# Optimization experiments

Hardware: AMD Instinct MI355X
Metric: run time of the kernel (lower is better)

Reference implementation:

```python
import jax, jax.numpy as jnp
import numpy as np

B, T, D, S, K = 4, 4096, 1024, 2048, 8

def _l2norm(v, axis=-1, eps=1e-12):
    # matches torch F.normalize: v / max(||v||, eps)
    n = jnp.sqrt(jnp.sum(v * v, axis=axis, keepdims=True))
    return v / jnp.maximum(n, eps)

def setup_inputs() -> dict:
    key = jax.random.key(0)
    ks = jax.random.split(key, 9)
    H = D // 2
    return {
        "x": jax.random.normal(ks[0], (B, T, D), dtype=jnp.float32),
        "memory_keys": jax.random.normal(ks[1], (S, D), dtype=jnp.float32) * 0.02,
        "memory_values": jax.random.normal(ks[2], (S, D), dtype=jnp.float32) * 0.02,
        "Wq": jax.random.normal(ks[3], (D, D), dtype=jnp.float32) * (1.0 / np.sqrt(D)),
        "Wo": jax.random.normal(ks[4], (D, D), dtype=jnp.float32) * (1.0 / np.sqrt(D)),
        "gW1": jax.random.normal(ks[5], (H, 2 * D), dtype=jnp.float32) * (1.0 / np.sqrt(2 * D)),
        "gb1": jnp.zeros((H,), dtype=jnp.float32),
        "gW2": jax.random.normal(ks[6], (1, H), dtype=jnp.float32) * (1.0 / np.sqrt(H)),
        "gb2": jnp.zeros((1,), dtype=jnp.float32),
    }

def reference(x, memory_keys, memory_values, Wq, Wo, gW1, gb1, gW2, gb2):
    # query projection (Linear, no bias): y = x @ W.T
    queries = jnp.einsum('btd,ed->bte', x, Wq)
    keys_norm = _l2norm(memory_keys)          # [S, D]
    queries_norm = _l2norm(queries)           # [B, T, D]
    # cosine similarities [B, T, S]
    sims = jnp.einsum('btd,sd->bts', queries_norm, keys_norm)
    topk_sims, topk_idx = jax.lax.top_k(sims, K)      # [B, T, K]
    topk_w = jax.nn.softmax(topk_sims, axis=-1)       # [B, T, K]
    topk_vals = memory_values[topk_idx]               # [B, T, K, D]
    retrieved = jnp.einsum('btk,btkd->btd', topk_w, topk_vals)
    retrieved = jnp.einsum('btd,ed->bte', retrieved, Wo)
    gate_in = jnp.concatenate([x, retrieved], axis=-1)           # [B, T, 2D]
    h = jax.nn.gelu(jnp.einsum('btc,hc->bth', gate_in, gW1) + gb1, approximate=False)
    gate = jax.nn.sigmoid(jnp.einsum('bth,oh->bto', h, gW2) + gb2)  # [B, T, 1]
    return x + gate * retrieved
```

## Files before the change

### kernel.cpp

```cpp
#include <hip/hip_runtime.h>
#include <math.h>

#define NROWS 16384
#define DDIM  1024
#define SKEYS 2048
#define KTOP  8
#define HDIM  512

typedef short  s16x8 __attribute__((ext_vector_type(8)));
typedef float  f32x4 __attribute__((ext_vector_type(4)));

#define GL16(g, l) __builtin_amdgcn_global_load_lds(                      \
    (const __attribute__((address_space(1))) void*)(g),                   \
    (__attribute__((address_space(3))) void*)(l), 16, 0, 0)

__device__ __forceinline__ float wave_sum(float v) {
#pragma unroll
    for (int off = 32; off > 0; off >>= 1) v += __shfl_xor(v, off, 64);
    return v;
}

__device__ __forceinline__ unsigned short f2bf(float f) {
    union { float f; unsigned u; } c; c.f = f;
    unsigned u = c.u;
    unsigned r = (u + 0x7FFFu + ((u >> 16) & 1u)) >> 16;
    return (unsigned short)r;
}

__device__ __forceinline__ float gelu_exact(float v) {
    return 0.5f * v * (1.0f + erff(v * 0.7071067811865475f));
}

__device__ __forceinline__ ushort4 cvt4(float4 v) {
    ushort4 o;
    o.x = f2bf(v.x); o.y = f2bf(v.y); o.z = f2bf(v.z); o.w = f2bf(v.w);
    return o;
}

__global__ __launch_bounds__(256) void prep_kernel(
        const float* __restrict__ x,   const float* __restrict__ Wq,
        const float* __restrict__ Wo,  const float* __restrict__ mv,
        const float* __restrict__ gW1, const float* __restrict__ mk,
        unsigned short* __restrict__ x_bf, unsigned short* __restrict__ bcat,
        unsigned short* __restrict__ wqT, unsigned short* __restrict__ wo_bf,
        unsigned short* __restrict__ mv_bf, unsigned short* __restrict__ gw1b,
        unsigned short* __restrict__ kn) {
    int bid = blockIdx.x, t = threadIdx.x;
    __shared__ float tlds[64][65];
    {
        float4 v = ((const float4*)(mk + (size_t)bid * DDIM))[t];
        float ss = v.x * v.x + v.y * v.y + v.z * v.z + v.w * v.w;
        ss = wave_sum(ss);
        __shared__ float wsum[4];
        if ((t & 63) == 0) wsum[t >> 6] = ss;
        __syncthreads();
        float tot = wsum[0] + wsum[1] + wsum[2] + wsum[3];
        float sc = 1.0f / fmaxf(sqrtf(tot), 1e-12f);
        float4 o = make_float4(v.x * sc, v.y * sc, v.z * sc, v.w * sc);
        ((ushort4*)(kn + (size_t)bid * DDIM))[t] = cvt4(o);
    }
    if (bid < 256) {
        int d0 = (bid >> 4) * 64, e0 = (bid & 15) * 64;
#pragma unroll
        for (int i = 0; i < 16; ++i) {
            int dr = i * 4 + (t >> 6);
            tlds[dr][t & 63] = Wq[(size_t)(d0 + dr) * DDIM + e0 + (t & 63)];
        }
        __syncthreads();
#pragma unroll
        for (int i = 0; i < 16; ++i) {
            int er = i * 4 + (t >> 6);
            wqT[(size_t)(e0 + er) * DDIM + d0 + (t & 63)] = f2bf(tlds[t & 63][er]);
        }
    }
    int gid = bid * 256 + t, stride = gridDim.x * 256;
    for (int i = gid; i < NROWS * DDIM / 4; i += stride)
        ((ushort4*)x_bf)[i] = cvt4(((const float4*)x)[i]);
    for (int i = gid; i < DDIM * DDIM / 4; i += stride)
        ((ushort4*)bcat)[524288 + i] = cvt4(((const float4*)Wq)[i]);
    for (int i = gid; i < HDIM * 2 * DDIM / 4; i += stride) {
        float4 v = ((const float4*)gW1)[i];
        int r = i >> 9, c4 = i & 511;
        if (c4 < 256) ((ushort4*)bcat)[786432 + r * 256 + c4] = cvt4(v);
        else          ((ushort4*)gw1b)[r * 256 + (c4 - 256)] = cvt4(v);
    }
    for (int i = gid; i < DDIM * DDIM / 4; i += stride)
        ((ushort4*)wo_bf)[i] = cvt4(((const float4*)Wo)[i]);
    for (int i = gid; i < SKEYS * DDIM / 4; i += stride)
        ((ushort4*)mv_bf)[i] = cvt4(((const float4*)mv)[i]);
}

struct GArg {
    const unsigned short* A;
    const unsigned short* B;
    unsigned short* C;
    unsigned short* C2;
    float* qpart;
    int Ncols, N2cols, nsplit, nsplit2, gx, nblocks, mode;
};

__global__ __launch_bounds__(256, 3) void dualgemm(GArg g0, GArg g1, int split) {
    __shared__ __align__(16) unsigned short As[2][4096];
    __shared__ __align__(16) unsigned short Bs[2][4096];

    int tid = threadIdx.x, l = tid & 63, wid = tid >> 6;
    bool first = ((int)blockIdx.x < split);
    GArg g = first ? g0 : g1;
    int bid = first ? blockIdx.x : blockIdx.x - split;
    int cpx = g.nblocks >> 3;
    int sbid = (bid & 7) * cpx + (bid >> 3);
    int m0 = (sbid / g.gx) * 128;
    int n0 = (sbid % g.gx) * 128;

    int wr = wid >> 1, wc = wid & 1;
    constexpr int NT = 32;

    f32x4 acc[4][4];
#pragma unroll
    for (int i = 0; i < 4; ++i)
#pragma unroll
        for (int j = 0; j < 4; ++j) acc[i][j] = (f32x4){0.f, 0.f, 0.f, 0.f};

    int srow   = tid >> 2;
    int schunk = (tid & 3) ^ ((srow >> 1) & 3);
    int offA[2], offB[2];
#pragma unroll
    for (int i = 0; i < 2; ++i) {
        offA[i] = (m0 + i * 64 + srow) * 1024;
        offB[i] = (n0 + i * 64 + srow) * 1024;
    }
    int ldsU = wid * 512;

#define STAGE(bsel, kt_)                                                       \
    do {                                                                       \
        int gk_ = (kt_) * 32 + schunk * 8;                                     \
        _Pragma("unroll")                                                      \
        for (int i_ = 0; i_ < 2; ++i_) {                                       \
            GL16(g.A + offA[i_] + gk_, &As[bsel][i_ * 2048 + ldsU]);           \
            GL16(g.B + offB[i_] + gk_, &Bs[bsel][i_ * 2048 + ldsU]);           \
        }                                                                      \
    } while (0)

    STAGE(0, 0);

    int frow = l & 15;
    int fp   = (l >> 4) ^ ((frow >> 1) & 3);
    int aoff = (wr * 64 + frow) * 32 + fp * 8;
    int boff = (wc * 64 + frow) * 32 + fp * 8;

#pragma unroll 2
    for (int kt = 0; kt < NT; ++kt) {
        int b = kt & 1;
        if (kt + 1 < NT) {
            STAGE(b ^ 1, kt + 1);
            asm volatile("s_waitcnt vmcnt(4)" ::: "memory");
        } else {
            asm volatile("s_waitcnt vmcnt(0)" ::: "memory");
        }
        __builtin_amdgcn_s_barrier();
        asm volatile("" ::: "memory");

        s16x8 af[4], bfr[4];
#pragma unroll
        for (int mf = 0; mf < 4; ++mf)
            af[mf] = *(const s16x8*)&As[b][aoff + mf * 512];
#pragma unroll
        for (int nf = 0; nf < 4; ++nf)
            bfr[nf] = *(const s16x8*)&Bs[b][boff + nf * 512];

        __builtin_amdgcn_s_setprio(1);
#pragma unroll
        for (int mf = 0; mf < 4; ++mf)
#pragma unroll
            for (int nf = 0; nf < 4; ++nf)
                acc[mf][nf] = __builtin_amdgcn_mfma_f32_16x16x32_bf16(
                    af[mf], bfr[nf], acc[mf][nf], 0, 0, 0);
        __builtin_amdgcn_s_setprio(0);
        asm volatile("" ::: "memory");
        __builtin_amdgcn_s_barrier();
        asm volatile("" ::: "memory");
    }
#undef STAGE

    int region = 0;
    unsigned short* cptr = g.C;
    int nc = g.Ncols, cb = n0;
    if (g.mode == 5) {
        if (n0 < g.nsplit) region = 1;
        else if (n0 < g.nsplit2) region = 2;
        else { region = 3; cptr = g.C2; nc = g.N2cols; cb = n0 - g.nsplit2; }
    }

    int crow = (l >> 4) << 2;
    int ccol = l & 15;
    if (region != 2) {
#pragma unroll
        for (int mf = 0; mf < 4; ++mf) {
            int gr = m0 + wr * 64 + mf * 16 + crow;
#pragma unroll
            for (int nf = 0; nf < 4; ++nf) {
                int gc = cb + wc * 64 + nf * 16 + ccol;
                f32x4 v = acc[mf][nf];
#pragma unroll
                for (int r2 = 0; r2 < 4; ++r2) {
                    unsigned short sv = f2bf(v[r2]);
                    if (region == 1)
                        sv = sv ^ ((sv & 0x8000) ? 0xFFFFu : 0x8000u);
                    cptr[(size_t)(gr + r2) * nc + gc] = sv;
                }
            }
        }
    } else {
        int slot = ((n0 - g.nsplit) >> 7) * 2 + wc;
#pragma unroll
        for (int mf = 0; mf < 4; ++mf)
#pragma unroll
            for (int r2 = 0; r2 < 4; ++r2) {
                float s = acc[mf][0][r2] * acc[mf][0][r2]
                        + acc[mf][1][r2] * acc[mf][1][r2]
                        + acc[mf][2][r2] * acc[mf][2][r2]
                        + acc[mf][3][r2] * acc[mf][3][r2];
                s += __shfl_xor(s, 1, 64);
                s += __shfl_xor(s, 2, 64);
                s += __shfl_xor(s, 4, 64);
                s += __shfl_xor(s, 8, 64);
                if ((l & 15) == 0)
                    g.qpart[(size_t)slot * NROWS +
                            (m0 + wr * 64 + mf * 16 + (l >> 4) * 4 + r2)] = s;
            }
    }
}

#define CED(k, i, j)                                                      \
    { unsigned mx_ = k[i] > k[j] ? k[i] : k[j];                           \
      unsigned mn_ = k[i] > k[j] ? k[j] : k[i];                           \
      k[i] = mx_; k[j] = mn_; }

__device__ __forceinline__ void sort8d(unsigned* k) {
    CED(k,0,1) CED(k,2,3) CED(k,4,5) CED(k,6,7)
    CED(k,0,2) CED(k,1,3) CED(k,4,6) CED(k,5,7)
    CED(k,1,2) CED(k,5,6)
    CED(k,0,4) CED(k,1,5) CED(k,2,6) CED(k,3,7)
    CED(k,2,4) CED(k,3,5)
    CED(k,1,2) CED(k,3,4) CED(k,5,6)
}

__device__ __forceinline__ void bclean8d(unsigned* t) {
    CED(t,0,4) CED(t,1,5) CED(t,2,6) CED(t,3,7)
    CED(t,0,2) CED(t,1,3) CED(t,4,6) CED(t,5,7)
    CED(t,0,1) CED(t,2,3) CED(t,4,5) CED(t,6,7)
}

__device__ __forceinline__ void merge8d(unsigned* a, const unsigned* b) {
    unsigned t[8];
#pragma unroll
    for (int i = 0; i < 8; ++i) t[i] = a[i] > b[7 - i] ? a[i] : b[7 - i];
    bclean8d(t);
#pragma unroll
    for (int i = 0; i < 8; ++i) a[i] = t[i];
}

__global__ __launch_bounds__(256) void mega_kernel(
        const float* __restrict__ qpart,
        const unsigned short* __restrict__ sims,
        const unsigned short* __restrict__ x_bf,
        const unsigned short* __restrict__ xg1,
        const unsigned short* __restrict__ mvo,
        const unsigned short* __restrict__ mvog,
        const float* __restrict__ gb1, const float* __restrict__ gW2,
        const float* __restrict__ gb2, float* __restrict__ out) {
    int wid = threadIdx.x >> 6, l = threadIdx.x & 63;
    int row = blockIdx.x * 4 + wid;

    const unsigned short* sr = sims + (size_t)row * SKEYS;
    uint4 raw0 = *(const uint4*)(sr + 0 * 512 + l * 8);
    uint4 raw1 = *(const uint4*)(sr + 1 * 512 + l * 8);
    uint4 raw2 = *(const uint4*)(sr + 2 * 512 + l * 8);
    uint4 raw3 = *(const uint4*)(sr + 3 * 512 + l * 8);
    const unsigned short* xr = x_bf + (size_t)row * DDIM + l * 16;
    uint4 x0 = *(const uint4*)xr, x1 = *(const uint4*)(xr + 8);
    uint4 xg = *(const uint4*)(xg1 + (size_t)row * HDIM + l * 8);

    float ssq = 0.f;
#pragma unroll
    for (int j = 0; j < 16; ++j) ssq += qpart[(size_t)j * NROWS + row];
    float qs = 1.0f / fmaxf(sqrtf(ssq), 1e-12f);

    unsigned key[32];
    {
        unsigned rw[16] = {raw0.x, raw0.y, raw0.z, raw0.w,
                           raw1.x, raw1.y, raw1.z, raw1.w,
                           raw2.x, raw2.y, raw2.z, raw2.w,
                           raw3.x, raw3.y, raw3.z, raw3.w};
#pragma unroll
        for (int c = 0; c < 4; ++c)
#pragma unroll
            for (int q2 = 0; q2 < 4; ++q2) {
                unsigned v = rw[c * 4 + q2];
                unsigned bi0 = (unsigned)(c * 512 + l * 8 + q2 * 2);
                key[c * 8 + q2 * 2]     = ((v & 0xFFFFu) << 16) | bi0;
                key[c * 8 + q2 * 2 + 1] = (v & 0xFFFF0000u) | (bi0 + 1);
            }
    }
    sort8d(key); sort8d(key + 8); sort8d(key + 16); sort8d(key + 24);
    merge8d(key, key + 8);
    merge8d(key + 16, key + 24);
    merge8d(key, key + 16);

#pragma unroll
    for (int off = 1; off <= 32; off <<= 1) {
        unsigned br[8];
#pragma unroll
        for (int i = 0; i < 8; ++i)
            br[i] = (unsigned)__shfl_xor((int)key[7 - i], off, 64);
        unsigned t[8];
#pragma unroll
        for (int i = 0; i < 8; ++i) t[i] = key[i] > br[i] ? key[i] : br[i];
        bclean8d(t);
#pragma unroll
        for (int i = 0; i < 8; ++i) key[i] = t[i];
    }

    float ov[8]; int oi[8];
#pragma unroll
    for (int j = 0; j < 8; ++j) {
        oi[j] = (int)(key[j] & 0xFFFFu);
        unsigned short ks = (unsigned short)(key[j] >> 16);
        unsigned short sv = ks ^ ((ks & 0x8000) ? 0x8000u : 0xFFFFu);
        ov[j] = __uint_as_float(((unsigned)sv) << 16);
    }
    float w[KTOP];
    float m = ov[0] * qs, ssum = 0.f;
#pragma unroll
    for (int j = 0; j < 8; ++j) { w[j] = expf(ov[j] * qs - m); ssum += w[j]; }
    float sinv = 1.0f / ssum;
#pragma unroll
    for (int j = 0; j < 8; ++j) w[j] *= sinv;

    float r2[16], hp[8];
#pragma unroll
    for (int j = 0; j < 16; ++j) r2[j] = 0.f;
#pragma unroll
    for (int j = 0; j < 8; ++j) hp[j] = 0.f;
#pragma unroll
    for (int k = 0; k < KTOP; ++k) {
        float wk = w[k];
        const unsigned short* mo = mvo + (size_t)oi[k] * DDIM + l * 16;
        uint4 a0 = *(const uint4*)mo;
        uint4 a1 = *(const uint4*)(mo + 8);
        const unsigned short* mg = mvog + (size_t)oi[k] * HDIM + l * 8;
        uint4 g0 = *(const uint4*)mg;
        unsigned aw[8] = {a0.x, a0.y, a0.z, a0.w, a1.x, a1.y, a1.z, a1.w};
#pragma unroll
        for (int j = 0; j < 8; ++j) {
            r2[2 * j]     += wk * __uint_as_float(aw[j] << 16);
            r2[2 * j + 1] += wk * __uint_as_float(aw[j] & 0xffff0000u);
        }
        unsigned gw[4] = {g0.x, g0.y, g0.z, g0.w};
#pragma unroll
        for (int j = 0; j < 4; ++j) {
            hp[2 * j]     += wk * __uint_as_float(gw[j] << 16);
            hp[2 * j + 1] += wk * __uint_as_float(gw[j] & 0xffff0000u);
        }
    }
    unsigned xgw[4] = {xg.x, xg.y, xg.z, xg.w};
    float p = 0.f;
#pragma unroll
    for (int j = 0; j < 4; ++j) {
        float h0 = gelu_exact(hp[2 * j] + __uint_as_float(xgw[j] << 16)
                              + gb1[l * 8 + 2 * j]);
        float h1 = gelu_exact(hp[2 * j + 1] + __uint_as_float(xgw[j] & 0xffff0000u)
                              + gb1[l * 8 + 2 * j + 1]);
        p += h0 * gW2[l * 8 + 2 * j] + h1 * gW2[l * 8 + 2 * j + 1];
    }
    p = wave_sum(p);
    float gate = 1.0f / (1.0f + expf(-(p + gb2[0])));
    unsigned xw[8] = {x0.x, x0.y, x0.z, x0.w, x1.x, x1.y, x1.z, x1.w};
    float o[16];
#pragma unroll
    for (int j = 0; j < 8; ++j) {
        o[2 * j]     = __uint_as_float(xw[j] << 16)         + gate * r2[2 * j];
        o[2 * j + 1] = __uint_as_float(xw[j] & 0xffff0000u) + gate * r2[2 * j + 1];
    }
    float4* po = (float4*)(out + (size_t)row * DDIM + l * 16);
    po[0] = make_float4(o[0], o[1], o[2], o[3]);
    po[1] = make_float4(o[4], o[5], o[6], o[7]);
    po[2] = make_float4(o[8], o[9], o[10], o[11]);
    po[3] = make_float4(o[12], o[13], o[14], o[15]);
}

extern "C" void kernel_launch(void* const* d_in, const int* in_sizes, int n_in,
                              void* d_out, int out_size, void* d_ws, size_t ws_size,
                              hipStream_t stream) {
    (void)in_sizes; (void)n_in; (void)out_size; (void)ws_size;
    const float* x   = (const float*)d_in[0];
    const float* mk  = (const float*)d_in[1];
    const float* mv  = (const float*)d_in[2];
    const float* Wq  = (const float*)d_in[3];
    const float* Wo  = (const float*)d_in[4];
    const float* gW1 = (const float*)d_in[5];
    const float* gb1 = (const float*)d_in[6];
    const float* gW2 = (const float*)d_in[7];
    const float* gb2 = (const float*)d_in[8];
    float* out = (float*)d_out;

    char* w = (char*)d_ws;
    unsigned short* x_bf    = (unsigned short*)w;  w += (size_t)NROWS * DDIM * 2;
    unsigned short* xg1_bf  = (unsigned short*)w;  w += (size_t)NROWS * HDIM * 2;
    unsigned short* kn_bf   = (unsigned short*)w;  w += (size_t)SKEYS * DDIM * 2;
    unsigned short* bcat    = (unsigned short*)w;  w += (size_t)3584 * DDIM * 2;
    unsigned short* wqT_bf  = (unsigned short*)w;  w += (size_t)DDIM * DDIM * 2;
    unsigned short* gw1b_bf = (unsigned short*)w;  w += (size_t)HDIM * DDIM * 2;
    unsigned short* wo_bf   = (unsigned short*)w;  w += (size_t)DDIM * DDIM * 2;
    unsigned short* mv_bf   = (unsigned short*)w;  w += (size_t)SKEYS * DDIM * 2;
    unsigned short* mvo_bf  = (unsigned short*)w;  w += (size_t)SKEYS * DDIM * 2;
    unsigned short* mvog_bf = (unsigned short*)w;  w += (size_t)SKEYS * HDIM * 2;
    unsigned short* sims    = (unsigned short*)w;  w += (size_t)NROWS * SKEYS * 2;
    float* qpart = (float*)w;                      w += (size_t)16 * NROWS * 4;

    prep_kernel<<<SKEYS, 256, 0, stream>>>(x, Wq, Wo, mv, gW1, mk,
                                           x_bf, bcat, wqT_bf, wo_bf, mv_bf,
                                           gw1b_bf, kn_bf);

    {
        GArg gk; gk.A = kn_bf; gk.B = wqT_bf; gk.C = bcat; gk.C2 = nullptr;
        gk.qpart = nullptr; gk.Ncols = DDIM; gk.N2cols = 0;
        gk.nsplit = 0; gk.nsplit2 = 0; gk.gx = 8; gk.nblocks = 128; gk.mode = 0;
        GArg gm; gm.A = mv_bf; gm.B = wo_bf; gm.C = mvo_bf; gm.C2 = nullptr;
        gm.qpart = nullptr; gm.Ncols = DDIM; gm.N2cols = 0;
        gm.nsplit = 0; gm.nsplit2 = 0; gm.gx = 8; gm.nblocks = 128; gm.mode = 0;
        dualgemm<<<256, 256, 0, stream>>>(gk, gm, 128);
    }

    {
        GArg gb; gb.A = x_bf; gb.B = bcat; gb.C = sims; gb.C2 = xg1_bf;
        gb.qpart = qpart; gb.Ncols = SKEYS; gb.N2cols = HDIM;
        gb.nsplit = 2048; gb.nsplit2 = 3072; gb.gx = 28; gb.nblocks = 3584; gb.mode = 5;
        GArg gg; gg.A = mvo_bf; gg.B = gw1b_bf; gg.C = mvog_bf; gg.C2 = nullptr;
        gg.qpart = nullptr; gg.Ncols = HDIM; gg.N2cols = 0;
        gg.nsplit = 0; gg.nsplit2 = 0; gg.gx = 4; gg.nblocks = 64; gg.mode = 0;
        dualgemm<<<3648, 256, 0, stream>>>(gb, gg, 3584);
    }

    mega_kernel<<<NROWS / 4, 256, 0, stream>>>(
        qpart, sims, x_bf, xg1_bf, mvo_bf, mvog_bf, gb1, gW2, gb2, out);
}
```

Baseline: 268.1 us.

## Enlarge GEMM tiles to 256x256 with 8 waves and triple-buffered LDS pipeline

The dual GEMM kernel moves from 128x128 tiles with 4 waves and double buffering to 256x256 tiles with 8 waves, each wave computing a 128x64 sub-tile. Loads are prefetched two k-steps ahead into a three-stage LDS ring, and the trailing barrier per iteration is removed. The aim is more operand reuse per byte loaded and better overlap of global loads with MFMA work. In exchange it uses more registers and LDS and occupancy drops to one block per CU. The small weight-prep GEMMs now launch very few blocks (64 and 16), which may underfill the GPU.

```diff
diff --git a/kernel.cpp b/kernel.cpp
--- a/kernel.cpp
+++ b/kernel.cpp
@@ -99,9 +99,9 @@
     int Ncols, N2cols, nsplit, nsplit2, gx, nblocks, mode;
 };
 
-__global__ __launch_bounds__(256, 3) void dualgemm(GArg g0, GArg g1, int split) {
-    __shared__ __align__(16) unsigned short As[2][4096];
-    __shared__ __align__(16) unsigned short Bs[2][4096];
+__global__ __launch_bounds__(512, 1) void dualgemm(GArg g0, GArg g1, int split) {
+    __shared__ __align__(16) unsigned short As[3 * 8192];
+    __shared__ __align__(16) unsigned short Bs[3 * 8192];
 
     int tid = threadIdx.x, l = tid & 63, wid = tid >> 6;
     bool first = ((int)blockIdx.x < split);
@@ -109,50 +109,48 @@
     int bid = first ? blockIdx.x : blockIdx.x - split;
     int cpx = g.nblocks >> 3;
     int sbid = (bid & 7) * cpx + (bid >> 3);
-    int m0 = (sbid / g.gx) * 128;
-    int n0 = (sbid % g.gx) * 128;
-
-    int wr = wid >> 1, wc = wid & 1;
+    int m0 = (sbid / g.gx) * 256;
+    int n0 = (sbid % g.gx) * 256;
+
+    int wm = wid >> 2, wn = wid & 3;
     constexpr int NT = 32;
 
-    f32x4 acc[4][4];
-#pragma unroll
-    for (int i = 0; i < 4; ++i)
+    f32x4 acc[8][4];
+#pragma unroll
+    for (int i = 0; i < 8; ++i)
 #pragma unroll
         for (int j = 0; j < 4; ++j) acc[i][j] = (f32x4){0.f, 0.f, 0.f, 0.f};
 
-    int srow   = tid >> 2;
-    int schunk = (tid & 3) ^ ((srow >> 1) & 3);
+    int srw = tid >> 2;
+    int sch = (tid & 3) ^ ((srw >> 1) & 3);
     int offA[2], offB[2];
 #pragma unroll
-    for (int i = 0; i < 2; ++i) {
-        offA[i] = (m0 + i * 64 + srow) * 1024;
-        offB[i] = (n0 + i * 64 + srow) * 1024;
+    for (int j = 0; j < 2; ++j) {
+        offA[j] = (m0 + j * 128 + srw) * 1024;
+        offB[j] = (n0 + j * 128 + srw) * 1024;
     }
     int ldsU = wid * 512;
 
-#define STAGE(bsel, kt_)                                                       \
+#define SPART(bsel, kt_, j_)                                                   \
     do {                                                                       \
-        int gk_ = (kt_) * 32 + schunk * 8;                                     \
-        _Pragma("unroll")                                                      \
-        for (int i_ = 0; i_ < 2; ++i_) {                                       \
-            GL16(g.A + offA[i_] + gk_, &As[bsel][i_ * 2048 + ldsU]);           \
-            GL16(g.B + offB[i_] + gk_, &Bs[bsel][i_ * 2048 + ldsU]);           \
-        }                                                                      \
+        int gk_ = (kt_) * 32 + sch * 8;                                        \
+        GL16(g.A + offA[j_] + gk_, &As[(bsel) * 8192 + (j_) * 4096 + ldsU]);   \
+        GL16(g.B + offB[j_] + gk_, &Bs[(bsel) * 8192 + (j_) * 4096 + ldsU]);   \
     } while (0)
-
-    STAGE(0, 0);
 
     int frow = l & 15;
     int fp   = (l >> 4) ^ ((frow >> 1) & 3);
-    int aoff = (wr * 64 + frow) * 32 + fp * 8;
-    int boff = (wc * 64 + frow) * 32 + fp * 8;
-
-#pragma unroll 2
+    int aoff = (wm * 128 + frow) * 32 + fp * 8;
+    int boff = (wn * 64 + frow) * 32 + fp * 8;
+
+    SPART(0, 0, 0); SPART(0, 0, 1);
+    SPART(1, 1, 0); SPART(1, 1, 1);
+
     for (int kt = 0; kt < NT; ++kt) {
-        int b = kt & 1;
+        int b = kt % 3;
+        int b2 = (kt + 2) % 3;
+        bool pf = (kt + 2 < NT);
         if (kt + 1 < NT) {
-            STAGE(b ^ 1, kt + 1);
             asm volatile("s_waitcnt vmcnt(4)" ::: "memory");
         } else {
             asm volatile("s_waitcnt vmcnt(0)" ::: "memory");
@@ -162,12 +160,12 @@
 
         s16x8 af[4], bfr[4];
 #pragma unroll
+        for (int nf = 0; nf < 4; ++nf)
+            bfr[nf] = *(const s16x8*)&Bs[b * 8192 + boff + nf * 512];
+#pragma unroll
         for (int mf = 0; mf < 4; ++mf)
-            af[mf] = *(const s16x8*)&As[b][aoff + mf * 512];
-#pragma unroll
-        for (int nf = 0; nf < 4; ++nf)
-            bfr[nf] = *(const s16x8*)&Bs[b][boff + nf * 512];
-
+            af[mf] = *(const s16x8*)&As[b * 8192 + aoff + mf * 512];
+        if (pf) SPART(b2, kt + 2, 0);
         __builtin_amdgcn_s_setprio(1);
 #pragma unroll
         for (int mf = 0; mf < 4; ++mf)
@@ -176,11 +174,22 @@
                 acc[mf][nf] = __builtin_amdgcn_mfma_f32_16x16x32_bf16(
                     af[mf], bfr[nf], acc[mf][nf], 0, 0, 0);
         __builtin_amdgcn_s_setprio(0);
+
+#pragma unroll
+        for (int mf = 0; mf < 4; ++mf)
+            af[mf] = *(const s16x8*)&As[b * 8192 + aoff + (mf + 4) * 512];
+        if (pf) SPART(b2, kt + 2, 1);
+        __builtin_amdgcn_s_setprio(1);
+#pragma unroll
+        for (int mf = 0; mf < 4; ++mf)
+#pragma unroll
+            for (int nf = 0; nf < 4; ++nf)
+                acc[mf + 4][nf] = __builtin_amdgcn_mfma_f32_16x16x32_bf16(
+                    af[mf], bfr[nf], acc[mf + 4][nf], 0, 0, 0);
+        __builtin_amdgcn_s_setprio(0);
         asm volatile("" ::: "memory");
-        __builtin_amdgcn_s_barrier();
-        asm volatile("" ::: "memory");
-    }
-#undef STAGE
+    }
+#undef SPART
 
     int region = 0;
     unsigned short* cptr = g.C;
@@ -195,11 +204,11 @@
     int ccol = l & 15;
     if (region != 2) {
 #pragma unroll
-        for (int mf = 0; mf < 4; ++mf) {
-            int gr = m0 + wr * 64 + mf * 16 + crow;
+        for (int mf = 0; mf < 8; ++mf) {
+            int gr = m0 + wm * 128 + mf * 16 + crow;
 #pragma unroll
             for (int nf = 0; nf < 4; ++nf) {
-                int gc = cb + wc * 64 + nf * 16 + ccol;
+                int gc = cb + wn * 64 + nf * 16 + ccol;
                 f32x4 v = acc[mf][nf];
 #pragma unroll
                 for (int r2 = 0; r2 < 4; ++r2) {
@@ -211,9 +220,9 @@
             }
         }
     } else {
-        int slot = ((n0 - g.nsplit) >> 7) * 2 + wc;
-#pragma unroll
-        for (int mf = 0; mf < 4; ++mf)
+        int slot = ((n0 - g.nsplit) >> 6) + wn;
+#pragma unroll
+        for (int mf = 0; mf < 8; ++mf)
 #pragma unroll
             for (int r2 = 0; r2 < 4; ++r2) {
                 float s = acc[mf][0][r2] * acc[mf][0][r2]
@@ -226,7 +235,7 @@
                 s += __shfl_xor(s, 8, 64);
                 if ((l & 15) == 0)
                     g.qpart[(size_t)slot * NROWS +
-                            (m0 + wr * 64 + mf * 16 + (l >> 4) * 4 + r2)] = s;
+                            (m0 + wm * 128 + mf * 16 + (l >> 4) * 4 + r2)] = s;
             }
     }
 }
@@ -425,21 +434,22 @@
     {
         GArg gk; gk.A = kn_bf; gk.B = wqT_bf; gk.C = bcat; gk.C2 = nullptr;
         gk.qpart = nullptr; gk.Ncols = DDIM; gk.N2cols = 0;
-        gk.nsplit = 0; gk.nsplit2 = 0; gk.gx = 8; gk.nblocks = 128; gk.mode = 0;
+        gk.nsplit = 0; gk.nsplit2 = 0; gk.gx = 4; gk.nblocks = 32; gk.mode = 0;
         GArg gm; gm.A = mv_bf; gm.B = wo_bf; gm.C = mvo_bf; gm.C2 = nullptr;
         gm.qpart = nullptr; gm.Ncols = DDIM; gm.N2cols = 0;
-        gm.nsplit = 0; gm.nsplit2 = 0; gm.gx = 8; gm.nblocks = 128; gm.mode = 0;
-        dualgemm<<<256, 256, 0, stream>>>(gk, gm, 128);
+        gm.nsplit = 0; gm.nsplit2 = 0; gm.gx = 4; gm.nblocks = 32; gm.mode = 0;
+        dualgemm<<<64, 512, 0, stream>>>(gk, gm, 32);
     }
 
     {
         GArg gb; gb.A = x_bf; gb.B = bcat; gb.C = sims; gb.C2 = xg1_bf;
         gb.qpart = qpart; gb.Ncols = SKEYS; gb.N2cols = HDIM;
-        gb.nsplit = 2048; gb.nsplit2 = 3072; gb.gx = 28; gb.nblocks = 3584; gb.mode = 5;
+        gb.nsplit = 2048; gb.nsplit2 = 3072; gb.gx = 14; gb.nblocks = 896;
+        gb.mode = 5;
         GArg gg; gg.A = mvo_bf; gg.B = gw1b_bf; gg.C = mvog_bf; gg.C2 = nullptr;
         gg.qpart = nullptr; gg.Ncols = HDIM; gg.N2cols = 0;
-        gg.nsplit = 0; gg.nsplit2 = 0; gg.gx = 4; gg.nblocks = 64; gg.mode = 0;
-        dualgemm<<<3648, 256, 0, stream>>>(gb, gg, 3584);
+        gg.nsplit = 0; gg.nsplit2 = 0; gg.gx = 2; gg.nblocks = 16; gg.mode = 0;
+        dualgemm<<<912, 512, 0, stream>>>(gb, gg, 896);
     }
 
     mega_kernel<<<NROWS / 4, 256, 0, stream>>>(
```

Measured after the change: 261.4 us. 2.5% less time.
